# Optimization experiments

Measured on AMD Instinct MI355X. Metric: run time of the kernel, lower is better.

The kernel has to match this reference:

```python
import jax, jax.numpy as jnp
import numpy as np

MESH_SIZE = 0.01
HID = 256
NUM_RES_LAYERS = 3
TEMP = 1e-3
M_SCALE_LO, M_SCALE_HI = 0.0, 10.0
OFF_LO, OFF_HI = -10.0, 10.0


def _triangle_mesh(step):
    # Preisach triangle: points (beta, alpha) with 0 <= beta <= alpha <= 1
    n = int(round(1.0 / step)) + 1
    g = np.linspace(0.0, 1.0, n).astype(np.float32)
    bb, aa = np.meshgrid(g, g, indexing='ij')
    sel = bb <= aa + 1e-9
    return np.stack([bb[sel], aa[sel]], axis=-1)  # [N, 2] (beta, alpha)


def _glorot(key, shape):
    fan = sum(shape)
    return jax.random.normal(key, shape, dtype=jnp.float32) * np.float32(np.sqrt(2.0 / fan))


def setup_inputs() -> dict:
    key = jax.random.key(0)
    ks = jax.random.split(key, 16)
    B, S, T = 16, 256, 1024
    inp = {
        'encoder_input': jax.random.normal(ks[0], (B, S, 2), dtype=jnp.float32),
        'decoder_input': jax.random.uniform(ks[1], (B, T, 1), dtype=jnp.float32),
        'encoder_mask': jnp.ones((B, S), dtype=jnp.float32),
        'base_mesh': jnp.asarray(_triangle_mesh(MESH_SIZE)),
        # density ResNetMLP params (2 -> HID -> ... -> 1)
        'dens_Win': _glorot(ks[2], (2, HID)),
        'dens_bin': jnp.zeros((HID,), jnp.float32),
        'dens_Wr': _glorot(ks[3], (NUM_RES_LAYERS, HID, HID)),
        'dens_br': jnp.zeros((NUM_RES_LAYERS, HID), jnp.float32),
        'dens_Wout': _glorot(ks[4], (HID, 1)),
        'dens_bout': jnp.zeros((1,), jnp.float32),
        # encoder params: sequence MLP + mesh/context fusion -> initial relay states
        'enc_Ws': _glorot(ks[5], (2, HID)),
        'enc_bs': jnp.zeros((HID,), jnp.float32),
        'enc_Wm': _glorot(ks[6], (3, HID)),
        'enc_Wc': _glorot(ks[7], (HID, HID)),
        'enc_bm': jnp.zeros((HID,), jnp.float32),
        'enc_Wo': _glorot(ks[8], (HID, 1)),
        'enc_bo': jnp.zeros((1,), jnp.float32),
        # constrained scalars (raw, sigmoid-interval transformed)
        'h_scale_raw': jnp.float32(0.0),
        'm_scale_raw': jnp.float32(0.0),
        'm_offset_raw': jnp.float32(0.0),
    }
    return inp


def _interval(raw, lo, hi):
    return lo + (hi - lo) * jax.nn.sigmoid(raw)


def reference(encoder_input, decoder_input, encoder_mask, base_mesh,
              dens_Win, dens_bin, dens_Wr, dens_br, dens_Wout, dens_bout,
              enc_Ws, enc_bs, enc_Wm, enc_Wc, enc_bm, enc_Wo, enc_bo,
              h_scale_raw, m_scale_raw, m_offset_raw):
    B = encoder_input.shape[0]
    mesh = jnp.broadcast_to(base_mesh[None], (B,) + base_mesh.shape)  # [B,N,2]
    # ---- density network (ResNetMLP + sigmoid, eval mode: dropout off)
    x = jax.nn.relu(mesh @ dens_Win + dens_bin)
    def res_block(h, wb):
        w, b = wb
        return h + jax.nn.relu(h @ w + b), None
    x, _ = jax.lax.scan(res_block, x, (dens_Wr, dens_br))
    density = jax.nn.sigmoid(x @ dens_Wout + dens_bout)[..., 0]  # [B,N]
    # ---- encoder: masked mean-pooled sequence context fused with mesh features
    seq = jax.nn.relu(encoder_input @ enc_Ws + enc_bs)  # [B,S,H]
    mask = encoder_mask[..., None]
    ctx = (seq * mask).sum(1) / jnp.maximum(mask.sum(1), 1.0)  # [B,H]
    mesh_feat = jnp.concatenate([mesh, density[..., None]], axis=-1)  # [B,N,3]
    z = jax.nn.relu(mesh_feat @ enc_Wm + (ctx @ enc_Wc)[:, None, :] + enc_bm)
    initial_states = jnp.tanh((z @ enc_Wo + enc_bo)[..., 0])  # [B,N] in [-1,1]
    # ---- soft Preisach relay scan over time
    beta = mesh[..., 0]   # [B,N]
    alpha = mesh[..., 1]  # [B,N]
    h = decoder_input[..., 0]  # [B,T]
    dsum = density.sum(-1)  # [B]
    def relay_step(s, h_t):  # s: [B,N], h_t: [B]
        ht = h_t[:, None]
        w_up = jax.nn.sigmoid((ht - alpha) / TEMP)   # push relay -> +1 when h >= alpha
        w_dn = jax.nn.sigmoid((beta - ht) / TEMP)    # push relay -> -1 when h <= beta
        s = s + w_up * (1.0 - s)
        s = s + w_dn * (-1.0 - s)
        m_t = (density * s).sum(-1) / dsum
        return s, m_t
    _, m_seq = jax.lax.scan(relay_step, initial_states, h.T)  # [T,B]
    m = m_seq.T  # [B,T]
    h_scale = _interval(h_scale_raw, M_SCALE_LO, M_SCALE_HI)
    m_scale = _interval(m_scale_raw, M_SCALE_LO, M_SCALE_HI)
    m_offset = _interval(m_offset_raw, OFF_LO, OFF_HI)
    b_out = h_scale * h + m_scale * m + m_offset
    return (b_out, density, m, initial_states, mesh)
```

## Files before the change

kernel.cpp:

```cpp
#include <hip/hip_runtime.h>
#include <hip/hip_bf16.h>
#include <math.h>

constexpr int kB = 16;
constexpr int kS = 256;
constexpr int kT = 1024;
constexpr int kM = 5151;
constexpr int kH = 256;
constexpr int kG = 16;
constexpr int kL = 64;
constexpr int kJW = 84;
constexpr int kJT = 16;
constexpr int kRB = 322;
constexpr float kSig = 1442.6950408889634f;
constexpr float kAiS = 14.426950408889634f;

constexpr int OFF_BOUT = 0;
constexpr int OFF_DENS = kB * kT;
constexpr int OFF_M    = OFF_DENS + kB * kM;
constexpr int OFF_IS   = OFF_M + kB * kT;
constexpr int OFF_MESH = OFF_IS + kB * kM;

constexpr int WS_TAB  = 0;
constexpr int WS_ISF  = 3489280;
constexpr int WS_PART = 3571712;
constexpr int WS_DENS = 4259840;
constexpr int WS_DENSP= 4265216;

__device__ __forceinline__ float exp2_fast(float x){ return __builtin_amdgcn_exp2f(x); }
__device__ __forceinline__ float rcp_fast(float x){ return __builtin_amdgcn_rcpf(x); }
__device__ __forceinline__ void wave_lds_fence(){
    asm volatile("s_waitcnt lgkmcnt(0)" ::: "memory");
}

__global__ __launch_bounds__(256) void k_tab(const float* __restrict__ dec,
        __hip_bfloat16* __restrict__ TAB){
    int t  = blockIdx.x * 256 + threadIdx.x;
    int ai = blockIdx.y;
    int b  = blockIdx.z;
    float hts = dec[b * kT + t] * kSig;
    float wu = rcp_fast(1.f + exp2_fast(fmaf((float)ai, kAiS, -hts)));
    TAB[(size_t)(b * 101 + ai) * kT + t] = __float2bfloat16(wu);
}

__global__ __launch_bounds__(256) void k_res3(const float* __restrict__ mesh,
        const float* __restrict__ Win, const float* __restrict__ bin,
        const float* __restrict__ Wr, const float* __restrict__ br,
        const float* __restrict__ Wout, float* __restrict__ dens_pre){
    __shared__ float xL[256 * 16];
    __shared__ float Wsh[32 * 256];
    __shared__ float dred[256];
    __shared__ float beL[16], alL[16];
    int t = threadIdx.x;
    int jl = t & 15, oo = t >> 4;
    int jb = blockIdx.x * kJT;
    if (t < 16){
        int jg = jb + t;
        beL[t] = (jg < kM) ? mesh[2*jg]   : 0.f;
        alL[t] = (jg < kM) ? mesh[2*jg+1] : 0.f;
    }
    __syncthreads();
    #pragma unroll
    for (int it = 0; it < 16; ++it){
        int lin = t + it * 256;
        int k = lin >> 4, j = lin & 15;
        xL[lin] = fmaxf(fmaf(beL[j], Win[k], fmaf(alL[j], Win[kH + k], bin[k])), 0.f);
    }
    for (int l = 0; l < 3; ++l){
        const float* W  = Wr + l * kH * kH;
        const float* bl = br + l * kH;
        float acc[16] = {};
        for (int ks = 0; ks < 8; ++ks){
            __syncthreads();
            const float4* Wg = (const float4*)(W + ks * 32 * kH);
            float4* Ws4 = (float4*)Wsh;
            #pragma unroll
            for (int it = 0; it < 8; ++it) Ws4[t + it * 256] = Wg[t + it * 256];
            __syncthreads();
            #pragma unroll 2
            for (int k = 0; k < 32; ++k){
                float xv = xL[(ks * 32 + k) * 16 + jl];
                const float4* wrow = (const float4*)&Wsh[k * 256 + oo * 16];
                float4 w0 = wrow[0], w1 = wrow[1], w2 = wrow[2], w3 = wrow[3];
                acc[ 0] = fmaf(xv, w0.x, acc[ 0]); acc[ 1] = fmaf(xv, w0.y, acc[ 1]);
                acc[ 2] = fmaf(xv, w0.z, acc[ 2]); acc[ 3] = fmaf(xv, w0.w, acc[ 3]);
                acc[ 4] = fmaf(xv, w1.x, acc[ 4]); acc[ 5] = fmaf(xv, w1.y, acc[ 5]);
                acc[ 6] = fmaf(xv, w1.z, acc[ 6]); acc[ 7] = fmaf(xv, w1.w, acc[ 7]);
                acc[ 8] = fmaf(xv, w2.x, acc[ 8]); acc[ 9] = fmaf(xv, w2.y, acc[ 9]);
                acc[10] = fmaf(xv, w2.z, acc[10]); acc[11] = fmaf(xv, w2.w, acc[11]);
                acc[12] = fmaf(xv, w3.x, acc[12]); acc[13] = fmaf(xv, w3.y, acc[13]);
                acc[14] = fmaf(xv, w3.z, acc[14]); acc[15] = fmaf(xv, w3.w, acc[15]);
            }
        }
        __syncthreads();
        #pragma unroll
        for (int i = 0; i < 16; ++i){
            int o = oo * 16 + i;
            float xo = xL[o * 16 + jl];
            xL[o * 16 + jl] = xo + fmaxf(acc[i] + bl[o], 0.f);
        }
    }
    float p = 0.f;
    #pragma unroll
    for (int i = 0; i < 16; ++i){
        int o = oo * 16 + i;
        p = fmaf(xL[o * 16 + jl], Wout[o], p);
    }
    dred[t] = p;
    __syncthreads();
    if (t < 16){
        float s = 0.f;
        #pragma unroll
        for (int ii = 0; ii < 16; ++ii) s += dred[ii * 16 + t];
        int jg = jb + t;
        if (jg < kM) dens_pre[jg] = s;
    }
}

__global__ __launch_bounds__(256) void k_init(const float* __restrict__ enc_in,
        const float* __restrict__ mask, const float* __restrict__ Ws,
        const float* __restrict__ bs, const float* __restrict__ Wc,
        const float* __restrict__ mesh, const float* __restrict__ dens_pre,
        const float* __restrict__ bout, const float* __restrict__ Wm,
        const float* __restrict__ bm, const float* __restrict__ Wo,
        const float* __restrict__ bo, float* __restrict__ dens,
        float* __restrict__ isf, float* __restrict__ out){
    __shared__ float ctx_l[kH];
    __shared__ float w0s[kH], w1s[kH], w2s[kH], bcs[kH], wos[kH];
    int tid = threadIdx.x;
    int b = blockIdx.y;
    {
        float w0 = Ws[tid], w1 = Ws[kH + tid], bh = bs[tid];
        float acc = 0.f, msum = 0.f;
        const float* e = enc_in + b * kS * 2;
        const float* mk = mask + b * kS;
        #pragma unroll 4
        for (int s = 0; s < kS; ++s){
            float e0 = e[2*s], e1 = e[2*s+1], mm = mk[s];
            float v = fmaxf(fmaf(e0, w0, fmaf(e1, w1, bh)), 0.f);
            acc = fmaf(v, mm, acc);
            msum += mm;
        }
        ctx_l[tid] = acc / fmaxf(msum, 1.f);
    }
    __syncthreads();
    float cw = 0.f;
    #pragma unroll 8
    for (int k = 0; k < kH; ++k) cw = fmaf(ctx_l[k], Wc[k * kH + tid], cw);
    w0s[tid] = Wm[tid];
    w1s[tid] = Wm[kH + tid];
    w2s[tid] = Wm[2*kH + tid];
    bcs[tid] = bm[tid] + cw;
    wos[tid] = Wo[tid];
    __syncthreads();
    int j = blockIdx.x * 256 + tid;
    if (j >= kM) return;
    float d = 1.f / (1.f + expf(-(dens_pre[j] + bout[0])));
    if (b == 0) dens[j] = d;
    float be = mesh[2*j], al = mesh[2*j+1];
    float acc = 0.f;
    #pragma unroll 8
    for (int h = 0; h < kH; ++h){
        float pre = fmaf(be, w0s[h], fmaf(al, w1s[h], fmaf(d, w2s[h], bcs[h])));
        acc = fmaf(fmaxf(pre, 0.f), wos[h], acc);
    }
    float s = tanhf(acc + bo[0]);
    isf[b * kM + j] = s;
    out[OFF_IS + b * kM + j] = s;
}

__device__ __forceinline__ float bfhalf(unsigned int w, int odd){
    return __uint_as_float(odd ? (w & 0xffff0000u) : (w << 16));
}

__global__ __launch_bounds__(64) void k_scan(const float* __restrict__ mesh,
        const float* __restrict__ dens, const float* __restrict__ isf,
        const __hip_bfloat16* __restrict__ TAB,
        __hip_bfloat16* __restrict__ partials, float* __restrict__ out){
    __shared__ unsigned short cb[kL * 66];
    int L = threadIdx.x;
    int blk = blockIdx.x;
    int xcd = blk & 7;
    int i   = blk >> 3;
    int b   = (xcd << 1) | (i >= kJW ? 1 : 0);
    int jw  = (i >= kJW) ? i - kJW : i;
    int j = jw * 64 + L;
    bool valid = j < kM;
    int jj = valid ? j : 0;
    float d  = valid ? dens[j] : 0.f;
    float q  = valid ? isf[b * kM + j] + 1.f : 0.f;
    float be = mesh[2*jj], al = mesh[2*jj+1];
    int ai = __float2int_rn(al * 100.f);
    int bi = __float2int_rn(be * 100.f);
    const __hip_bfloat16* ra = TAB + (size_t)(b * 101 + ai) * kT;
    const __hip_bfloat16* rb = TAB + (size_t)(b * 101 + bi) * kT;
    if (valid){
        out[OFF_DENS + b * kM + j] = d;
        out[OFF_MESH + 2 * (b * kM + j)]     = be;
        out[OFF_MESH + 2 * (b * kM + j) + 1] = al;
    }
    size_t pbase = (size_t)(b * kJW + jw) * kT + L;

    unsigned int uaA[32], ubA[32], uaB[32], ubB[32];

    auto load_chunk = [&](int g, unsigned int* UA, unsigned int* UB){
        const uint4* pa = (const uint4*)(ra + g * kL);
        const uint4* pb = (const uint4*)(rb + g * kL);
        #pragma unroll
        for (int i2 = 0; i2 < 8; ++i2){
            uint4 va = pa[i2];
            UA[4*i2]=va.x; UA[4*i2+1]=va.y; UA[4*i2+2]=va.z; UA[4*i2+3]=va.w;
        }
        #pragma unroll
        for (int i2 = 0; i2 < 8; ++i2){
            uint4 vb = pb[i2];
            UB[4*i2]=vb.x; UB[4*i2+1]=vb.y; UB[4*i2+2]=vb.z; UB[4*i2+3]=vb.w;
        }
    };
    auto compute_chunk = [&](int g, const unsigned int* UA, const unsigned int* UB){
        #pragma unroll
        for (int t = 0; t < kL; ++t){
            float u = bfhalf(UA[t>>1], t & 1);
            float w = bfhalf(UB[t>>1], t & 1);
            q = w * fmaf(u, 2.f - q, q);
            float v = fmaf(d, q, -d);
            cb[t * 66 + L] = (unsigned short)(__float_as_uint(v) >> 16);
        }
        wave_lds_fence();
        float a0 = 0.f, a1 = 0.f;
        const __hip_bfloat162* row = (const __hip_bfloat162*)&cb[L * 66];
        #pragma unroll
        for (int i2 = 0; i2 < 32; ++i2){
            float2 f = __bfloat1622float2(row[i2]);
            a0 += f.x; a1 += f.y;
        }
        partials[pbase + g * kL] = __float2bfloat16(a0 + a1);
        wave_lds_fence();
    };

    load_chunk(0, uaA, ubA);
    #pragma unroll 1
    for (int g = 0; g < kG; g += 2){
        load_chunk(g + 1, uaB, ubB);
        compute_chunk(g, uaA, ubA);
        if (g + 2 < kG) load_chunk(g + 2, uaA, ubA);
        compute_chunk(g + 1, uaB, ubB);
    }
}

__global__ __launch_bounds__(256) void k_final(const __hip_bfloat16* __restrict__ partials,
        const float* __restrict__ dens, const float* __restrict__ dec,
        const float* __restrict__ hsr, const float* __restrict__ msr,
        const float* __restrict__ mor, float* __restrict__ out){
    __shared__ float red[4];
    int tid = threadIdx.x;
    int b = blockIdx.y;
    float ds = 0.f;
    for (int i = tid; i < kM; i += 256) ds += dens[i];
    #pragma unroll
    for (int off = 32; off; off >>= 1) ds += __shfl_down(ds, off, 64);
    if ((tid & 63) == 0) red[tid >> 6] = ds;
    __syncthreads();
    float dsum = red[0] + red[1] + red[2] + red[3];
    int t = blockIdx.x * 256 + tid;
    float acc = 0.f;
    const __hip_bfloat16* p = partials + (size_t)b * kJW * kT + t;
    #pragma unroll 4
    for (int w = 0; w < kJW; ++w) acc += __bfloat162float(p[(size_t)w * kT]);
    float m = acc / dsum;
    float hscale = 10.f / (1.f + expf(-hsr[0]));
    float mscale = 10.f / (1.f + expf(-msr[0]));
    float moff   = -10.f + 20.f / (1.f + expf(-mor[0]));
    float h = dec[b * kT + t];
    out[OFF_M + b * kT + t]    = m;
    out[OFF_BOUT + b * kT + t] = fmaf(hscale, h, fmaf(mscale, m, moff));
}

extern "C" void kernel_launch(void* const* d_in, const int* in_sizes, int n_in,
                              void* d_out, int out_size, void* d_ws, size_t ws_size,
                              hipStream_t stream) {
    (void)in_sizes; (void)n_in; (void)out_size; (void)ws_size;
    const float* enc_in = (const float*)d_in[0];
    const float* dec    = (const float*)d_in[1];
    const float* mask   = (const float*)d_in[2];
    const float* mesh   = (const float*)d_in[3];
    const float* Win    = (const float*)d_in[4];
    const float* bin    = (const float*)d_in[5];
    const float* Wr     = (const float*)d_in[6];
    const float* br     = (const float*)d_in[7];
    const float* Wout   = (const float*)d_in[8];
    const float* bout   = (const float*)d_in[9];
    const float* Ws     = (const float*)d_in[10];
    const float* bs     = (const float*)d_in[11];
    const float* Wm     = (const float*)d_in[12];
    const float* Wc     = (const float*)d_in[13];
    const float* bm     = (const float*)d_in[14];
    const float* Wo     = (const float*)d_in[15];
    const float* bo     = (const float*)d_in[16];
    const float* hsr    = (const float*)d_in[17];
    const float* msr    = (const float*)d_in[18];
    const float* mor    = (const float*)d_in[19];
    float* out = (float*)d_out;

    float* ws = (float*)d_ws;
    __hip_bfloat16* TAB      = (__hip_bfloat16*)(ws + WS_TAB);
    float* isf   = ws + WS_ISF;
    __hip_bfloat16* partials = (__hip_bfloat16*)(ws + WS_PART);
    float* densv = ws + WS_DENS;
    float* densp = ws + WS_DENSP;

    k_tab   <<<dim3(4, 101, kB),  256, 0, stream>>>(dec, TAB);
    k_res3  <<<dim3(kRB),         256, 0, stream>>>(mesh, Win, bin, Wr, br, Wout, densp);
    k_init  <<<dim3(21, kB),      256, 0, stream>>>(enc_in, mask, Ws, bs, Wc, mesh, densp,
                                                    bout, Wm, bm, Wo, bo, densv, isf, out);
    k_scan  <<<dim3(kJW * kB),     64, 0, stream>>>(mesh, densv, isf, TAB, partials, out);
    k_final <<<dim3(4, kB),       256, 0, stream>>>(partials, densv, dec, hsr, msr, mor, out);
}
```

Measured before the change: 246.5 us.

## Restructure density MLP kernel into per-wave tiles with direct global weight reads

Reworks the residual-MLP density kernel so that each wave owns four mesh points and each lane owns four output channels. Activations stay in padded LDS rows that only the owning wave touches, so block-wide barriers become wave-local LDS fences. Weights are read straight from global memory (through the cache) instead of being staged into shared memory in chunks. The final projection uses wave shuffles instead of an LDS reduction. This removes barrier and staging overhead, but each wave now re-reads the full weight matrix from cache, and each weight load is reused across only four points instead of sixteen.

```diff
diff --git a/kernel.cpp b/kernel.cpp
--- a/kernel.cpp
+++ b/kernel.cpp
@@ -47,73 +47,90 @@
         const float* __restrict__ Win, const float* __restrict__ bin,
         const float* __restrict__ Wr, const float* __restrict__ br,
         const float* __restrict__ Wout, float* __restrict__ dens_pre){
-    __shared__ float xL[256 * 16];
-    __shared__ float Wsh[32 * 256];
-    __shared__ float dred[256];
-    __shared__ float beL[16], alL[16];
+    __shared__ float xL[kJT * 264];
     int t = threadIdx.x;
-    int jl = t & 15, oo = t >> 4;
+    int og = t & 63;
+    int jg = t >> 6;
     int jb = blockIdx.x * kJT;
-    if (t < 16){
-        int jg = jb + t;
-        beL[t] = (jg < kM) ? mesh[2*jg]   : 0.f;
-        alL[t] = (jg < kM) ? mesh[2*jg+1] : 0.f;
-    }
-    __syncthreads();
+    int o0 = og * 4;
+    float be[4], al[4];
     #pragma unroll
-    for (int it = 0; it < 16; ++it){
-        int lin = t + it * 256;
-        int k = lin >> 4, j = lin & 15;
-        xL[lin] = fmaxf(fmaf(beL[j], Win[k], fmaf(alL[j], Win[kH + k], bin[k])), 0.f);
-    }
+    for (int i = 0; i < 4; ++i){
+        int jglob = jb + jg * 4 + i;
+        bool v = jglob < kM;
+        be[i] = v ? mesh[2*jglob]   : 0.f;
+        al[i] = v ? mesh[2*jglob+1] : 0.f;
+    }
+    {
+        float4 w0 = *(const float4*)&Win[o0];
+        float4 w1 = *(const float4*)&Win[kH + o0];
+        float4 b0 = *(const float4*)&bin[o0];
+        #pragma unroll
+        for (int i = 0; i < 4; ++i){
+            float4 x;
+            x.x = fmaxf(fmaf(be[i], w0.x, fmaf(al[i], w1.x, b0.x)), 0.f);
+            x.y = fmaxf(fmaf(be[i], w0.y, fmaf(al[i], w1.y, b0.y)), 0.f);
+            x.z = fmaxf(fmaf(be[i], w0.z, fmaf(al[i], w1.z, b0.z)), 0.f);
+            x.w = fmaxf(fmaf(be[i], w0.w, fmaf(al[i], w1.w, b0.w)), 0.f);
+            *(float4*)&xL[(jg * 4 + i) * 264 + o0] = x;
+        }
+    }
+    wave_lds_fence();
     for (int l = 0; l < 3; ++l){
         const float* W  = Wr + l * kH * kH;
         const float* bl = br + l * kH;
-        float acc[16] = {};
-        for (int ks = 0; ks < 8; ++ks){
-            __syncthreads();
-            const float4* Wg = (const float4*)(W + ks * 32 * kH);
-            float4* Ws4 = (float4*)Wsh;
+        float acc[4][4] = {};
+        #pragma unroll 2
+        for (int k = 0; k < kH; k += 4){
+            float4 xv[4];
             #pragma unroll
-            for (int it = 0; it < 8; ++it) Ws4[t + it * 256] = Wg[t + it * 256];
-            __syncthreads();
-            #pragma unroll 2
-            for (int k = 0; k < 32; ++k){
-                float xv = xL[(ks * 32 + k) * 16 + jl];
-                const float4* wrow = (const float4*)&Wsh[k * 256 + oo * 16];
-                float4 w0 = wrow[0], w1 = wrow[1], w2 = wrow[2], w3 = wrow[3];
-                acc[ 0] = fmaf(xv, w0.x, acc[ 0]); acc[ 1] = fmaf(xv, w0.y, acc[ 1]);
-                acc[ 2] = fmaf(xv, w0.z, acc[ 2]); acc[ 3] = fmaf(xv, w0.w, acc[ 3]);
-                acc[ 4] = fmaf(xv, w1.x, acc[ 4]); acc[ 5] = fmaf(xv, w1.y, acc[ 5]);
-                acc[ 6] = fmaf(xv, w1.z, acc[ 6]); acc[ 7] = fmaf(xv, w1.w, acc[ 7]);
-                acc[ 8] = fmaf(xv, w2.x, acc[ 8]); acc[ 9] = fmaf(xv, w2.y, acc[ 9]);
-                acc[10] = fmaf(xv, w2.z, acc[10]); acc[11] = fmaf(xv, w2.w, acc[11]);
-                acc[12] = fmaf(xv, w3.x, acc[12]); acc[13] = fmaf(xv, w3.y, acc[13]);
-                acc[14] = fmaf(xv, w3.z, acc[14]); acc[15] = fmaf(xv, w3.w, acc[15]);
+            for (int i = 0; i < 4; ++i)
+                xv[i] = *(const float4*)&xL[(jg * 4 + i) * 264 + k];
+            #pragma unroll
+            for (int kk = 0; kk < 4; ++kk){
+                float4 w = *(const float4*)&W[(k + kk) * kH + o0];
+                #pragma unroll
+                for (int i = 0; i < 4; ++i){
+                    float xs = kk == 0 ? xv[i].x : kk == 1 ? xv[i].y
+                             : kk == 2 ? xv[i].z : xv[i].w;
+                    acc[i][0] = fmaf(xs, w.x, acc[i][0]);
+                    acc[i][1] = fmaf(xs, w.y, acc[i][1]);
+                    acc[i][2] = fmaf(xs, w.z, acc[i][2]);
+                    acc[i][3] = fmaf(xs, w.w, acc[i][3]);
+                }
             }
         }
-        __syncthreads();
-        #pragma unroll
-        for (int i = 0; i < 16; ++i){
-            int o = oo * 16 + i;
-            float xo = xL[o * 16 + jl];
-            xL[o * 16 + jl] = xo + fmaxf(acc[i] + bl[o], 0.f);
-        }
-    }
-    float p = 0.f;
+        wave_lds_fence();
+        float4 bb = *(const float4*)&bl[o0];
+        #pragma unroll
+        for (int i = 0; i < 4; ++i){
+            float4 xo = *(const float4*)&xL[(jg * 4 + i) * 264 + o0];
+            xo.x += fmaxf(acc[i][0] + bb.x, 0.f);
+            xo.y += fmaxf(acc[i][1] + bb.y, 0.f);
+            xo.z += fmaxf(acc[i][2] + bb.z, 0.f);
+            xo.w += fmaxf(acc[i][3] + bb.w, 0.f);
+            *(float4*)&xL[(jg * 4 + i) * 264 + o0] = xo;
+        }
+        wave_lds_fence();
+    }
+    float4 wo = *(const float4*)&Wout[o0];
+    float p[4];
     #pragma unroll
-    for (int i = 0; i < 16; ++i){
-        int o = oo * 16 + i;
-        p = fmaf(xL[o * 16 + jl], Wout[o], p);
-    }
-    dred[t] = p;
-    __syncthreads();
-    if (t < 16){
-        float s = 0.f;
-        #pragma unroll
-        for (int ii = 0; ii < 16; ++ii) s += dred[ii * 16 + t];
-        int jg = jb + t;
-        if (jg < kM) dens_pre[jg] = s;
+    for (int i = 0; i < 4; ++i){
+        float4 x = *(const float4*)&xL[(jg * 4 + i) * 264 + o0];
+        p[i] = fmaf(x.x, wo.x, fmaf(x.y, wo.y, fmaf(x.z, wo.z, x.w * wo.w)));
+    }
+    #pragma unroll
+    for (int off = 32; off; off >>= 1){
+        #pragma unroll
+        for (int i = 0; i < 4; ++i) p[i] += __shfl_down(p[i], off, 64);
+    }
+    if (og == 0){
+        #pragma unroll
+        for (int i = 0; i < 4; ++i){
+            int jglob = jb + jg * 4 + i;
+            if (jglob < kM) dens_pre[jglob] = p[i];
+        }
     }
 }
 
```

Measured after the change: 249.5 us. Within noise of the previous version (+1.2%).
